# Kernel optimization log

Hardware: AMD Instinct MI355X
Metric: run time of the kernel (lower is better)

Reference implementation:

```python
import jax, jax.numpy as jnp
import numpy as np

T = 2048          # total nodes across all sub-batches
NUM_SEG = 64      # scenes
SEG = T // NUM_SEG
F_DIM = 32
H_DIM = 128
FEAT_DIM = 4


def setup_inputs() -> dict:
    key = jax.random.key(0)
    k1, k2, k3, k4, k5, k6 = jax.random.split(key, 6)
    f = jax.random.normal(k1, (T, T, F_DIM), dtype=jnp.float32)
    h = jax.random.normal(k2, (T, H_DIM), dtype=jnp.float32)
    # features[:, :, 0] is pairwise distance; uniform [0, 20] so d > 10 masks ~half
    features = jax.random.uniform(k3, (T, T, FEAT_DIM), dtype=jnp.float32) * 20.0
    # horizontal bearing angles; ~N(0,1) so theta < 0 masks ~half
    hor_bearings_MTX = jax.random.normal(k4, (T, T), dtype=jnp.float32)
    # nn.Linear(h_dim, f_dim): weight [f_dim, h_dim], bias [f_dim]
    W_w = jax.random.normal(k5, (F_DIM, H_DIM), dtype=jnp.float32) / np.sqrt(H_DIM)
    W_b = jax.random.normal(k6, (F_DIM,), dtype=jnp.float32) * 0.01
    starts = jnp.arange(NUM_SEG, dtype=jnp.int64) * SEG
    sub_batches = jnp.stack([starts, starts + SEG], axis=1)  # [NUM_SEG, 2]
    return {"f": f, "h": h, "features": features,
            "hor_bearings_MTX": hor_bearings_MTX,
            "W_w": W_w, "W_b": W_b, "sub_batches": sub_batches}


def reference(f, h, features, hor_bearings_MTX, W_w, W_b, sub_batches):
    n = h.shape[0]
    distance = features[:, :, 0]                      # [T, T]
    Wh = h @ W_w.T + W_b                              # [T, f_dim]
    # sigma[i, j] = f[i, j, :] . Wh[j, :]
    logits = jnp.einsum('ijf,jf->ij', f, Wh)          # [T, T]
    starts = sub_batches[:, 0]
    seg_size = sub_batches[:, 1] - sub_batches[:, 0]
    seg_id = jnp.searchsorted(starts, jnp.arange(n), side='right') - 1  # [T]
    same_seg = seg_id[:, None] == seg_id[None, :]
    self_mask = jnp.eye(n, dtype=bool)
    # within-segment gated entries are set to -1000 (as in the original),
    # cross-segment entries are excluded from the softmax entirely
    bad = (hor_bearings_MTX < 0) | (distance > 10.0) | self_mask
    masked = jnp.where(same_seg,
                       jnp.where(bad, jnp.float32(-1000.0), logits),
                       -jnp.inf)
    attn = jax.nn.softmax(masked, axis=1)             # [T, T]
    S = attn @ h                                      # [T, h_dim]
    # segments of size 1 are skipped in the original (S stays zero)
    size_per_node = seg_size[seg_id]
    S = jnp.where((size_per_node > 1)[:, None], S, jnp.float32(0.0))
    return S
```

## Files before the change

kernel.cpp:

```cpp
#include <hip/hip_runtime.h>


#define TT 2048
#define SEG 32
#define FD 32
#define HD 128

__global__ __launch_bounds__(256) void horizon_attn_kernel(
    const float* __restrict__ f, const float* __restrict__ h,
    const float* __restrict__ features, const float* __restrict__ hor,
    const float* __restrict__ Ww, const float* __restrict__ Wb,
    float* __restrict__ out)
{
    __shared__ float sh_h[SEG][HD];
    __shared__ float sh_Wh[SEG][FD + 1];
    __shared__ float sh_attn[8][SEG];

    const int tid = threadIdx.x;
    const int seg = blockIdx.x >> 2;
    const int rowBase = seg * SEG + (blockIdx.x & 3) * 8;
    const int j0 = seg * SEG;

    {
        const float4* hseg = (const float4*)(h + (size_t)j0 * HD);
        float4* shh4 = (float4*)&sh_h[0][0];
        for (int v = tid; v < (SEG * HD) / 4; v += 256) shh4[v] = hseg[v];
    }
    __syncthreads();

    for (int v = tid; v < SEG * FD; v += 256) {
        const int jj = v >> 5, ff = v & 31;
        const float* wrow = Ww + ff * HD;
        const float* hrow = sh_h[jj];
        float acc = 0.f;
        #pragma unroll 8
        for (int d = 0; d < HD; ++d) acc += hrow[d] * wrow[d];
        sh_Wh[jj][ff] = acc + Wb[ff];
    }
    __syncthreads();

    const int r  = tid >> 5;
    const int jj = tid & 31;
    const int i  = rowBase + r;
    const int j  = j0 + jj;

    const float* frow = f + ((size_t)i * TT + j) * FD;
    float logit = 0.f;
    #pragma unroll
    for (int k = 0; k < FD; k += 4) {
        const float4 fv = *(const float4*)(frow + k);
        logit += fv.x * sh_Wh[jj][k]     + fv.y * sh_Wh[jj][k + 1]
               + fv.z * sh_Wh[jj][k + 2] + fv.w * sh_Wh[jj][k + 3];
    }

    const float dist = features[((size_t)i * TT + j) * 4];
    const float hb   = hor[(size_t)i * TT + j];
    const bool bad = (hb < 0.f) | (dist > 10.f) | (i == j);
    const float m = bad ? -1000.f : logit;

    float mx = m;
    #pragma unroll
    for (int mask = 16; mask; mask >>= 1) mx = fmaxf(mx, __shfl_xor(mx, mask));
    const float e = __expf(m - mx);
    float s = e;
    #pragma unroll
    for (int mask = 16; mask; mask >>= 1) s += __shfl_xor(s, mask);
    sh_attn[r][jj] = e / s;
    __syncthreads();

    const int d0 = jj * 4;
    float4 acc = make_float4(0.f, 0.f, 0.f, 0.f);
    #pragma unroll 8
    for (int q = 0; q < SEG; ++q) {
        const float a = sh_attn[r][q];
        const float4 hv = *(const float4*)&sh_h[q][d0];
        acc.x += a * hv.x; acc.y += a * hv.y;
        acc.z += a * hv.z; acc.w += a * hv.w;
    }
    *(float4*)(out + (size_t)i * HD + d0) = acc;
}

extern "C" void kernel_launch(void* const* d_in, const int* in_sizes, int n_in,
                              void* d_out, int out_size, void* d_ws, size_t ws_size,
                              hipStream_t stream) {
    const float* f        = (const float*)d_in[0];
    const float* h        = (const float*)d_in[1];
    const float* features = (const float*)d_in[2];
    const float* hor      = (const float*)d_in[3];
    const float* Ww       = (const float*)d_in[4];
    const float* Wb       = (const float*)d_in[5];
    float* out = (float*)d_out;

    hipLaunchKernelGGL(horizon_attn_kernel, dim3(256), dim3(256), 0, stream,
                       f, h, features, hor, Ww, Wb, out);
}
```

Measured before the change: 623.6 us.

## Precompute Wh in separate kernel and prefetch f row before shared-memory staging

Moves the h@W^T+b projection into its own small kernel that writes to workspace, so the attention blocks no longer recompute a 32x128x32 matvec per block before loading data. The attention kernel now issues its global loads of f, distance and bearing first, then stages h and the precomputed Wh into shared memory, overlapping the long-latency loads with staging. Wh rows are padded to 36 floats so they can be read as float4. This adds a second launch and a workspace round trip.

```diff
diff --git a/kernel.cpp b/kernel.cpp
--- a/kernel.cpp
+++ b/kernel.cpp
@@ -6,14 +6,31 @@
 #define FD 32
 #define HD 128
 
+__global__ __launch_bounds__(256) void wh_kernel(
+    const float* __restrict__ h, const float* __restrict__ Ww,
+    const float* __restrict__ Wb, float* __restrict__ wh)
+{
+    const int t  = blockIdx.x * 8 + (threadIdx.x >> 5);
+    const int ff = threadIdx.x & 31;
+    const float4* hrow = (const float4*)(h + (size_t)t * HD);
+    const float4* wrow = (const float4*)(Ww + (size_t)ff * HD);
+    float acc = 0.f;
+    #pragma unroll
+    for (int q = 0; q < HD / 4; ++q) {
+        const float4 a = hrow[q];
+        const float4 b = wrow[q];
+        acc += a.x * b.x + a.y * b.y + a.z * b.z + a.w * b.w;
+    }
+    wh[(size_t)t * FD + ff] = acc + Wb[ff];
+}
+
 __global__ __launch_bounds__(256) void horizon_attn_kernel(
     const float* __restrict__ f, const float* __restrict__ h,
     const float* __restrict__ features, const float* __restrict__ hor,
-    const float* __restrict__ Ww, const float* __restrict__ Wb,
-    float* __restrict__ out)
+    const float* __restrict__ wh, float* __restrict__ out)
 {
     __shared__ float sh_h[SEG][HD];
-    __shared__ float sh_Wh[SEG][FD + 1];
+    __shared__ float sh_Wh[SEG][FD + 4];
     __shared__ float sh_attn[8][SEG];
 
     const int tid = threadIdx.x;
@@ -21,40 +38,38 @@
     const int rowBase = seg * SEG + (blockIdx.x & 3) * 8;
     const int j0 = seg * SEG;
 
-    {
-        const float4* hseg = (const float4*)(h + (size_t)j0 * HD);
-        float4* shh4 = (float4*)&sh_h[0][0];
-        for (int v = tid; v < (SEG * HD) / 4; v += 256) shh4[v] = hseg[v];
-    }
-    __syncthreads();
-
-    for (int v = tid; v < SEG * FD; v += 256) {
-        const int jj = v >> 5, ff = v & 31;
-        const float* wrow = Ww + ff * HD;
-        const float* hrow = sh_h[jj];
-        float acc = 0.f;
-        #pragma unroll 8
-        for (int d = 0; d < HD; ++d) acc += hrow[d] * wrow[d];
-        sh_Wh[jj][ff] = acc + Wb[ff];
-    }
-    __syncthreads();
-
     const int r  = tid >> 5;
     const int jj = tid & 31;
     const int i  = rowBase + r;
     const int j  = j0 + jj;
 
     const float* frow = f + ((size_t)i * TT + j) * FD;
+    float4 fv[8];
+    #pragma unroll
+    for (int k = 0; k < 8; ++k) fv[k] = *(const float4*)(frow + 4 * k);
+    const float dist = features[((size_t)i * TT + j) * 4];
+    const float hb   = hor[(size_t)i * TT + j];
+
+    {
+        const float4* hseg = (const float4*)(h + (size_t)j0 * HD);
+        float4* shh4 = (float4*)&sh_h[0][0];
+        #pragma unroll
+        for (int v = tid; v < (SEG * HD) / 4; v += 256) shh4[v] = hseg[v];
+
+        const float4 wv = ((const float4*)(wh + (size_t)j0 * FD))[tid];
+        const int wjj = tid >> 3, wkq = tid & 7;
+        *(float4*)&sh_Wh[wjj][wkq * 4] = wv;
+    }
+    __syncthreads();
+
     float logit = 0.f;
     #pragma unroll
     for (int k = 0; k < FD; k += 4) {
-        const float4 fv = *(const float4*)(frow + k);
-        logit += fv.x * sh_Wh[jj][k]     + fv.y * sh_Wh[jj][k + 1]
-               + fv.z * sh_Wh[jj][k + 2] + fv.w * sh_Wh[jj][k + 3];
+        const float4 wq = *(const float4*)&sh_Wh[jj][k];
+        const float4 fq = fv[k >> 2];
+        logit += fq.x * wq.x + fq.y * wq.y + fq.z * wq.z + fq.w * wq.w;
     }
 
-    const float dist = features[((size_t)i * TT + j) * 4];
-    const float hb   = hor[(size_t)i * TT + j];
     const bool bad = (hb < 0.f) | (dist > 10.f) | (i == j);
     const float m = bad ? -1000.f : logit;
 
@@ -90,7 +105,10 @@
     const float* Ww       = (const float*)d_in[4];
     const float* Wb       = (const float*)d_in[5];
     float* out = (float*)d_out;
+    float* wh  = (float*)d_ws;
 
+    hipLaunchKernelGGL(wh_kernel, dim3(TT / 8), dim3(256), 0, stream,
+                       h, Ww, Wb, wh);
     hipLaunchKernelGGL(horizon_attn_kernel, dim3(256), dim3(256), 0, stream,
-                       f, h, features, hor, Ww, Wb, out);
+                       f, h, features, hor, wh, out);
 }
```

After: 612.6 us. No clear change (-1.8%).
